# Kernel optimization log

Measured on AMD Instinct MI355X. Metric: run time of the kernel, lower is better.

Reference implementation:

```python
import jax, jax.numpy as jnp
import numpy as np
from jax import lax

H, I, N, R, K, B, L = 2048, 4096, 16, 128, 4, 1, 2048

def silu(v):
    return v * jax.nn.sigmoid(v)

def setup_inputs() -> dict:
    key = jax.random.key(0)
    ks = jax.random.split(key, 8)
    f = jnp.float32
    x = jax.random.normal(ks[0], (B, L, H), f)
    W_in = jax.random.normal(ks[1], (H, 2 * I), f) / np.sqrt(H).astype(np.float32)
    conv_w = jax.random.normal(ks[2], (I, 1, K), f) / np.sqrt(K).astype(np.float32)  # OIH depthwise
    conv_b = jnp.zeros((I,), f)
    W_x = jax.random.normal(ks[3], (I, R + 2 * N), f) / np.sqrt(I).astype(np.float32)
    W_dt = jax.random.normal(ks[4], (R, I), f) / np.sqrt(R).astype(np.float32)
    # dt bias init as in Mamba: inverse-softplus of log-uniform dt
    dt = jnp.clip(jnp.exp(jax.random.normal(ks[5], (I,), f) * (np.log(0.1) - np.log(0.001)).astype(np.float32) + np.float32(np.log(0.001))), 1e-4, 0.1)
    b_dt = dt + jnp.log(-jnp.expm1(-dt))
    W_out = jax.random.normal(ks[6], (I, H), f) / np.sqrt(I).astype(np.float32)
    A_log = jnp.log(jnp.broadcast_to(jnp.arange(1, N + 1, dtype=f), (I, N)))
    D = jnp.ones((I,), f)
    return {"x": x, "W_in": W_in, "conv_w": conv_w, "conv_b": conv_b, "W_x": W_x,
            "W_dt": W_dt, "b_dt": b_dt, "W_out": W_out, "A_log": A_log, "D": D}

def reference(x, W_in, conv_w, conv_b, W_x, W_dt, b_dt, W_out, A_log, D):
    Bsz, Lq, _ = x.shape
    proj = jnp.swapaxes(x @ W_in, 1, 2)            # [B, 2I, L]
    h, gate = jnp.split(proj, 2, axis=1)           # each [B, I, L]
    # depthwise causal conv1d (pad K-1 both sides, truncate to L)
    h = lax.conv_general_dilated(h, conv_w, (1,), ((K - 1, K - 1),), feature_group_count=I)[..., :Lq]
    h = silu(h + conv_b[None, :, None])            # [B, I, L]
    ssm = jnp.swapaxes(h, 1, 2) @ W_x              # [B, L, R+2N]
    dt, Bm, Cm = jnp.split(ssm, [R, R + N], axis=-1)
    dt = jax.nn.softplus(dt @ W_dt + b_dt)         # [B, L, I]
    dt = jnp.swapaxes(dt, 1, 2)                    # [B, I, L]
    A = -jnp.exp(A_log)                            # [I, N]
    dA = jnp.exp(A[None, :, None, :] * dt[..., None])          # [B, I, L, N]
    dBu = dt[..., None] * Bm[:, None, :, :] * h[..., None]     # [B, I, L, N]

    def step(s, inp):
        dA_t, dBu_t, C_t = inp                     # [B,I,N],[B,I,N],[B,N]
        s = dA_t * s + dBu_t
        y = jnp.einsum('bin,bn->bi', s, C_t)
        return s, y

    s0 = jnp.zeros((Bsz, I, N), x.dtype)
    _, ys = lax.scan(step, s0, (jnp.moveaxis(dA, 2, 0), jnp.moveaxis(dBu, 2, 0), jnp.swapaxes(Cm, 0, 1)))
    y = jnp.moveaxis(ys, 0, 2)                     # [B, I, L]
    y = (y + h * D[None, :, None]) * silu(gate)
    return jnp.swapaxes(y, 1, 2) @ W_out           # [B, L, H]
```

## Files before the change

kernel.cpp:

```cpp
#include <hip/hip_runtime.h>

typedef unsigned short u16;
typedef unsigned int u32;
typedef __attribute__((ext_vector_type(2))) float f32x2;
typedef __attribute__((ext_vector_type(4))) float f32x4;
typedef __attribute__((ext_vector_type(8))) short s16x8;
typedef __attribute__((ext_vector_type(4))) u16 u16x4;

static constexpr int Hdim = 2048, Idim = 4096, Ndim = 16, Rdim = 128, Lseq = 2048;
static constexpr int NCH = 64, LCH = 32;

__device__ __forceinline__ u16 f2bf(float f) {
  u32 u = __builtin_bit_cast(u32, f);
  u += 0x7fffu + ((u >> 16) & 1u);
  return (u16)(u >> 16);
}
__device__ __forceinline__ float bf2f(u16 u) {
  u32 x = ((u32)u) << 16;
  return __builtin_bit_cast(float, x);
}

__global__ void k_cvt(const float* __restrict__ src, u16* __restrict__ dst, int n4) {
  int i = blockIdx.x * blockDim.x + threadIdx.x;
  if (i >= n4) return;
  f32x4 v = ((const f32x4*)src)[i];
  u16x4 o = {f2bf(v.x), f2bf(v.y), f2bf(v.z), f2bf(v.w)};
  ((u16x4*)dst)[i] = o;
}

__global__ void k_tcvt(const float* __restrict__ src, u16* __restrict__ dst,
                       int R, int C, int dstld) {
  __shared__ float tile[32][33];
  int tx = threadIdx.x & 31, ty = threadIdx.x >> 5;
  int c0 = blockIdx.x * 32, r0 = blockIdx.y * 32;
#pragma unroll
  for (int j = 0; j < 32; j += 8) {
    int r = r0 + ty + j, c = c0 + tx;
    tile[ty + j][tx] = (r < R && c < C) ? src[(size_t)r * C + c] : 0.f;
  }
  __syncthreads();
#pragma unroll
  for (int j = 0; j < 32; j += 8) {
    int c = c0 + ty + j, r = r0 + tx;
    if (c < C && r < R) dst[(size_t)c * dstld + r] = f2bf(tile[tx][ty + j]);
  }
}

__global__ __launch_bounds__(256)
void k_tcvt64(const float* __restrict__ src, u16* __restrict__ dst, int C, int ld) {
  __shared__ u16 tile[64][68];
  const int c0 = blockIdx.x * 64, r0 = blockIdx.y * 64;
#pragma unroll
  for (int it = 0; it < 4; ++it) {
    int v = it * 256 + threadIdx.x;
    int row = v >> 4, c4 = v & 15;
    f32x4 d = *(const f32x4*)&src[(size_t)(r0 + row) * C + c0 + c4 * 4];
    u16x4 o = {f2bf(d.x), f2bf(d.y), f2bf(d.z), f2bf(d.w)};
    *(u16x4*)&tile[row][c4 * 4] = o;
  }
  __syncthreads();
#pragma unroll
  for (int it = 0; it < 4; ++it) {
    int v = it * 256 + threadIdx.x;
    int oc = v >> 4, r4 = v & 15;
    u16x4 o = {tile[r4 * 4 + 0][oc], tile[r4 * 4 + 1][oc],
               tile[r4 * 4 + 2][oc], tile[r4 * 4 + 3][oc]};
    *(u16x4*)&dst[(size_t)(c0 + oc) * ld + r0 + r4 * 4] = o;
  }
}

__global__ void k_conv(const u16* __restrict__ projb, const float* __restrict__ cw,
                       const float* __restrict__ cb, u16* __restrict__ hcb) {
  int idx = blockIdx.x * 256 + threadIdx.x;
  int i = idx & (Idim - 1), l = idx >> 12;
  float acc = cb[i];
#pragma unroll
  for (int k = 0; k < 4; ++k) {
    int lk = l - 3 + k;
    if (lk >= 0) acc += cw[i * 4 + k] * bf2f(projb[(size_t)lk * (2 * Idim) + i]);
  }
  float s = acc * (1.f / (1.f + __expf(-acc)));
  hcb[idx] = f2bf(s);
}

__global__ void k_dtr(const float* __restrict__ ssm, u16* __restrict__ dtr) {
  int i = blockIdx.x * blockDim.x + threadIdx.x;
  int l = i >> 5, c4 = i & 31;
  f32x4 v = *(const f32x4*)&ssm[(size_t)l * 256 + c4 * 4];
  u16x4 o = {f2bf(v.x), f2bf(v.y), f2bf(v.z), f2bf(v.w)};
  *(u16x4*)&dtr[(size_t)l * 128 + c4 * 4] = o;
}

__global__ __launch_bounds__(256)
void k_scan1(const float* __restrict__ dtf, const u16* __restrict__ hcb,
             const float* __restrict__ ssm, const float* __restrict__ A_log,
             float* __restrict__ Sloc, float* __restrict__ dtsum) {
  __shared__ float Bs[LCH][16];
  const int c = blockIdx.y;
  const int i = blockIdx.x * 256 + threadIdx.x;
  const int l0 = c * LCH;
  {
    int t = threadIdx.x;
    int l = t >> 3, q = t & 7;
    *(f32x2*)&Bs[l][q * 2] = *(const f32x2*)&ssm[(size_t)(l0 + l) * 256 + 128 + q * 2];
  }
  float a[16];
#pragma unroll
  for (int n4 = 0; n4 < 4; ++n4) {
    f32x4 v = *(const f32x4*)&A_log[(size_t)i * 16 + n4 * 4];
    a[n4 * 4 + 0] = -__expf(v.x);
    a[n4 * 4 + 1] = -__expf(v.y);
    a[n4 * 4 + 2] = -__expf(v.z);
    a[n4 * 4 + 3] = -__expf(v.w);
  }
  __syncthreads();
  float s[16];
#pragma unroll
  for (int n = 0; n < 16; ++n) s[n] = 0.f;
  float dsum = 0.f;
  for (int l = 0; l < LCH; ++l) {
    float dtv = dtf[(size_t)(l0 + l) * Idim + i];
    float hv = bf2f(hcb[(size_t)(l0 + l) * Idim + i]);
    dsum += dtv;
    float dh = dtv * hv;
#pragma unroll
    for (int n = 0; n < 16; ++n) {
      float dA = __expf(a[n] * dtv);
      s[n] = dA * s[n] + dh * Bs[l][n];
    }
  }
#pragma unroll
  for (int n4 = 0; n4 < 4; ++n4) {
    f32x4 v = {s[n4 * 4], s[n4 * 4 + 1], s[n4 * 4 + 2], s[n4 * 4 + 3]};
    *(f32x4*)&Sloc[((size_t)c * Idim + i) * 16 + n4 * 4] = v;
  }
  dtsum[(size_t)c * Idim + i] = dsum;
}

__global__ __launch_bounds__(256)
void k_scan2(const float* __restrict__ Sloc, const float* __restrict__ dtsum,
             const float* __restrict__ A_log, float* __restrict__ sinit) {
  const int idx = blockIdx.x * 256 + threadIdx.x;
  const float a = -__expf(A_log[idx]);
  const int i = idx >> 4;
  float acc = 0.f;
  for (int c = 0; c < NCH; ++c) {
    size_t o = (size_t)c * (Idim * 16) + idx;
    sinit[o] = acc;
    acc = __expf(a * dtsum[(size_t)c * Idim + i]) * acc + Sloc[o];
  }
}

__global__ __launch_bounds__(256)
void k_scan3(const float* __restrict__ dtf, const u16* __restrict__ hcb,
             const float* __restrict__ ssm, const float* __restrict__ A_log,
             const float* __restrict__ Dp, const u16* __restrict__ projb,
             const float* __restrict__ sinit, u16* __restrict__ yb) {
  __shared__ float SBC[LCH][32];
  const int c = blockIdx.y;
  const int i = blockIdx.x * 256 + threadIdx.x;
  const int l0 = c * LCH;
  {
    int t = threadIdx.x;
    int l = t >> 3, q = t & 7;
    *(f32x4*)&SBC[l][q * 4] = *(const f32x4*)&ssm[(size_t)(l0 + l) * 256 + 128 + q * 4];
  }
  float a[16], s[16];
#pragma unroll
  for (int n4 = 0; n4 < 4; ++n4) {
    f32x4 v = *(const f32x4*)&A_log[(size_t)i * 16 + n4 * 4];
    a[n4 * 4 + 0] = -__expf(v.x);
    a[n4 * 4 + 1] = -__expf(v.y);
    a[n4 * 4 + 2] = -__expf(v.z);
    a[n4 * 4 + 3] = -__expf(v.w);
    f32x4 sv = *(const f32x4*)&sinit[((size_t)c * Idim + i) * 16 + n4 * 4];
    s[n4 * 4 + 0] = sv.x;
    s[n4 * 4 + 1] = sv.y;
    s[n4 * 4 + 2] = sv.z;
    s[n4 * 4 + 3] = sv.w;
  }
  const float Di = Dp[i];
  __syncthreads();
  for (int l = 0; l < LCH; ++l) {
    float dtv = dtf[(size_t)(l0 + l) * Idim + i];
    float hv = bf2f(hcb[(size_t)(l0 + l) * Idim + i]);
    float dh = dtv * hv;
    float y = 0.f;
#pragma unroll
    for (int n = 0; n < 16; ++n) {
      float dA = __expf(a[n] * dtv);
      s[n] = dA * s[n] + dh * SBC[l][n];
      y += s[n] * SBC[l][16 + n];
    }
    float g = bf2f(projb[(size_t)(l0 + l) * (2 * Idim) + Idim + i]);
    y = (y + hv * Di) * (g / (1.f + __expf(-g)));
    yb[(size_t)(l0 + l) * Idim + i] = f2bf(y);
  }
}

__device__ __forceinline__ void gload_lds16(const void* g, void* l) {
  __builtin_amdgcn_global_load_lds((const __attribute__((address_space(1))) void*)g,
                                   (__attribute__((address_space(3))) void*)l, 16, 0, 0);
}

template <int EPI>
__device__ __forceinline__ void gemm_body(const u16* __restrict__ A, const u16* __restrict__ Bt,
                                          float* __restrict__ C, u16* __restrict__ Caux,
                                          int N, int K, int kchunk,
                                          const float* __restrict__ bias,
                                          int m0, int n0, int kz) {
  __shared__ u16 As[128 * 32];
  __shared__ u16 Bs[128 * 32];
  const int tid = threadIdx.x;
  const int wave = tid >> 6, lane = tid & 63;
  const int wm = (wave >> 1) * 64, wn = (wave & 1) * 64;
  const int lr = lane >> 2;
  const int lc = lane & 3;
  const int arow = wave * 32;

  f32x4 acc[4][4];
#pragma unroll
  for (int a = 0; a < 4; ++a)
#pragma unroll
    for (int b = 0; b < 4; ++b) acc[a][b] = (f32x4){0.f, 0.f, 0.f, 0.f};

  const int k_begin = kz * kchunk;
  const int k_end = k_begin + kchunk;

  for (int k = k_begin; k < k_end; k += 32) {
#pragma unroll
    for (int j = 0; j < 2; ++j) {
      const u16* ga = A + (size_t)(m0 + arow + j * 16 + lr) * K + k + lc * 8;
      gload_lds16(ga, &As[(arow + j * 16) * 32]);
      const u16* gb = Bt + (size_t)(n0 + arow + j * 16 + lr) * K + k + lc * 8;
      gload_lds16(gb, &Bs[(arow + j * 16) * 32]);
    }
    __syncthreads();
    const int kh = (lane >> 4) * 8;
    const int fr = lane & 15;
    s16x8 af[4], bfr[4];
#pragma unroll
    for (int f = 0; f < 4; ++f) {
      af[f] = *(const s16x8*)&As[(wm + f * 16 + fr) * 32 + kh];
      bfr[f] = *(const s16x8*)&Bs[(wn + f * 16 + fr) * 32 + kh];
    }
#pragma unroll
    for (int fm = 0; fm < 4; ++fm)
#pragma unroll
      for (int fn = 0; fn < 4; ++fn)
        acc[fm][fn] = __builtin_amdgcn_mfma_f32_16x16x32_bf16(af[fm], bfr[fn], acc[fm][fn], 0, 0, 0);
    __syncthreads();
  }

  const int cr = (lane >> 4) * 4, cc = lane & 15;
#pragma unroll
  for (int fm = 0; fm < 4; ++fm)
#pragma unroll
    for (int fn = 0; fn < 4; ++fn)
#pragma unroll
      for (int j = 0; j < 4; ++j) {
        int row = m0 + wm + fm * 16 + cr + j;
        int col = n0 + wn + fn * 16 + cc;
        float v = acc[fm][fn][j];
        if (EPI == 0) {
          C[(size_t)row * N + col] = v;
        } else if (EPI == 1) {
          atomicAdd(&C[(size_t)row * N + col], v);
        } else if (EPI == 2) {
          float xv = v + bias[col];
          C[(size_t)row * N + col] = fmaxf(xv, 0.f) + log1pf(__expf(-fabsf(xv)));
        } else {
          Caux[(size_t)row * N + col] = f2bf(v);
        }
      }
}

__global__ __launch_bounds__(256)
void k_gemm1(const u16* __restrict__ A, const u16* __restrict__ Bt, u16* __restrict__ Caux) {
  int bid = blockIdx.x;
  int wg = (bid & 7) * 128 + (bid >> 3);
  int m0 = (wg & 15) * 128, n0 = (wg >> 4) * 128;
  gemm_body<4>(A, Bt, nullptr, Caux, 2 * Idim, Hdim, Hdim, nullptr, m0, n0, 0);
}

__global__ __launch_bounds__(256)
void k_gemm3(const u16* __restrict__ A, const u16* __restrict__ Bt, float* __restrict__ C) {
  gemm_body<1>(A, Bt, C, nullptr, 256, Idim, Idim / 8, nullptr,
               blockIdx.x * 128, blockIdx.y * 128, blockIdx.z);
}

__global__ __launch_bounds__(256)
void k_gemm4(const u16* __restrict__ A, const u16* __restrict__ Bt, float* __restrict__ C,
             const float* __restrict__ bias) {
  gemm_body<2>(A, Bt, C, nullptr, Idim, Rdim, Rdim, bias,
               blockIdx.x * 128, blockIdx.y * 128, 0);
}

__global__ __launch_bounds__(256)
void k_gemm5(const u16* __restrict__ A, const u16* __restrict__ Bt, float* __restrict__ C) {
  int bid = blockIdx.x;
  int wg = (bid & 7) * 32 + (bid >> 3);
  int m0 = (wg & 15) * 128, n0 = (wg >> 4) * 128;
  gemm_body<1>(A, Bt, C, nullptr, Hdim, Idim, Idim / 2, nullptr, m0, n0, blockIdx.y);
}

extern "C" void kernel_launch(void* const* d_in, const int* in_sizes, int n_in,
                              void* d_out, int out_size, void* d_ws, size_t ws_size,
                              hipStream_t stream) {
  const float* x = (const float*)d_in[0];
  const float* W_in = (const float*)d_in[1];
  const float* convw = (const float*)d_in[2];
  const float* convb = (const float*)d_in[3];
  const float* W_x = (const float*)d_in[4];
  const float* W_dt = (const float*)d_in[5];
  const float* b_dt = (const float*)d_in[6];
  const float* W_out = (const float*)d_in[7];
  const float* A_log = (const float*)d_in[8];
  const float* Dp = (const float*)d_in[9];
  float* out = (float*)d_out;

  char* w = (char*)d_ws;
  const size_t OFF_PROJ = 0;
  const size_t OFF_HC = OFF_PROJ + (size_t)Lseq * 2 * Idim * 4;
  const size_t OFF_DT = OFF_HC + (size_t)Lseq * Idim * 4;
  const size_t OFF_XB = OFF_DT + (size_t)Lseq * Idim * 4;
  const size_t OFF_WIN = OFF_XB + (size_t)Lseq * Hdim * 2;
  const size_t OFF_WOUT = OFF_WIN + (size_t)2 * Idim * Hdim * 2;
  const size_t OFF_HCB = OFF_WOUT + (size_t)Hdim * Idim * 2;
  const size_t OFF_YB = OFF_HCB + (size_t)Lseq * Idim * 2;
  const size_t OFF_WX = OFF_YB + (size_t)Lseq * Idim * 2;
  const size_t OFF_WDT = OFF_WX + (size_t)256 * Idim * 2;
  const size_t OFF_SSM = OFF_WDT + (size_t)Idim * Rdim * 2;
  const size_t OFF_DTR = OFF_SSM + (size_t)Lseq * 256 * 4;

  u16* projb = (u16*)(w + OFF_PROJ);
  float* dtf = (float*)(w + OFF_DT);
  u16* xb = (u16*)(w + OFF_XB);
  u16* winT = (u16*)(w + OFF_WIN);
  u16* woutT = (u16*)(w + OFF_WOUT);
  u16* hcb = (u16*)(w + OFF_HCB);
  u16* yb = (u16*)(w + OFF_YB);
  u16* wxt = (u16*)(w + OFF_WX);
  u16* wdtT = (u16*)(w + OFF_WDT);
  float* ssm = (float*)(w + OFF_SSM);
  u16* dtr = (u16*)(w + OFF_DTR);
  float* Sloc = (float*)(w + OFF_HC);
  float* sinit = (float*)(w + OFF_WIN);
  float* dtsum = (float*)(w + OFF_WIN + (size_t)16 * 1024 * 1024);

  hipMemsetAsync(wxt, 0, (size_t)256 * Idim * 2, stream);
  hipMemsetAsync(ssm, 0, (size_t)Lseq * 256 * 4, stream);
  hipMemsetAsync(out, 0, (size_t)Lseq * Hdim * 4, stream);

  k_cvt<<<(Lseq * Hdim / 4 + 255) / 256, 256, 0, stream>>>(x, xb, Lseq * Hdim / 4);
  k_tcvt64<<<dim3(2 * Idim / 64, Hdim / 64), 256, 0, stream>>>(W_in, winT, 2 * Idim, Hdim);
  k_tcvt<<<dim3(5, Idim / 32), 256, 0, stream>>>(W_x, wxt, Idim, 160, Idim);
  k_tcvt64<<<dim3(Idim / 64, Rdim / 64), 256, 0, stream>>>(W_dt, wdtT, Idim, Rdim);
  k_tcvt64<<<dim3(Hdim / 64, Idim / 64), 256, 0, stream>>>(W_out, woutT, Hdim, Idim);

  k_gemm1<<<1024, 256, 0, stream>>>(xb, winT, projb);

  k_conv<<<(size_t)Lseq * Idim / 256, 256, 0, stream>>>(projb, convw, convb, hcb);

  k_gemm3<<<dim3(Lseq / 128, 2, 8), 256, 0, stream>>>(hcb, wxt, ssm);

  k_dtr<<<Lseq * 32 / 256, 256, 0, stream>>>(ssm, dtr);

  k_gemm4<<<dim3(Lseq / 128, Idim / 128), 256, 0, stream>>>(dtr, wdtT, dtf, b_dt);

  k_scan1<<<dim3(Idim / 256, NCH), 256, 0, stream>>>(dtf, hcb, ssm, A_log, Sloc, dtsum);
  k_scan2<<<Idim * 16 / 256, 256, 0, stream>>>(Sloc, dtsum, A_log, sinit);
  k_scan3<<<dim3(Idim / 256, NCH), 256, 0, stream>>>(dtf, hcb, ssm, A_log, Dp, projb, sinit, yb);

  k_gemm5<<<dim3(256, 2), 256, 0, stream>>>(yb, woutT, out);
}
```

Baseline: 514.0 us.

## Replace input-projection GEMM with 256x256 eight-wave pipelined kernel; store dt as bf16

Replaces the 128x128 input-projection GEMM with a 512-thread, 256x256-tile kernel. It uses 128 KB of dynamic LDS, double-buffered half-tile staging via global_load_lds, interleaved barriers and MFMA priority hints, so loads overlap compute and operands are reused more. It also makes the dt projection epilogue write softplus output as bf16, and the scan kernels read it as bf16, halving that traffic at some precision cost. Two memsets are merged into one covering the contiguous W_x and ssm regions.

```diff
diff --git a/kernel.cpp b/kernel.cpp
--- a/kernel.cpp
+++ b/kernel.cpp
@@ -92,7 +92,7 @@
 }
 
 __global__ __launch_bounds__(256)
-void k_scan1(const float* __restrict__ dtf, const u16* __restrict__ hcb,
+void k_scan1(const u16* __restrict__ dtfb, const u16* __restrict__ hcb,
              const float* __restrict__ ssm, const float* __restrict__ A_log,
              float* __restrict__ Sloc, float* __restrict__ dtsum) {
   __shared__ float Bs[LCH][16];
@@ -119,7 +119,7 @@
   for (int n = 0; n < 16; ++n) s[n] = 0.f;
   float dsum = 0.f;
   for (int l = 0; l < LCH; ++l) {
-    float dtv = dtf[(size_t)(l0 + l) * Idim + i];
+    float dtv = bf2f(dtfb[(size_t)(l0 + l) * Idim + i]);
     float hv = bf2f(hcb[(size_t)(l0 + l) * Idim + i]);
     dsum += dtv;
     float dh = dtv * hv;
@@ -152,7 +152,7 @@
 }
 
 __global__ __launch_bounds__(256)
-void k_scan3(const float* __restrict__ dtf, const u16* __restrict__ hcb,
+void k_scan3(const u16* __restrict__ dtfb, const u16* __restrict__ hcb,
              const float* __restrict__ ssm, const float* __restrict__ A_log,
              const float* __restrict__ Dp, const u16* __restrict__ projb,
              const float* __restrict__ sinit, u16* __restrict__ yb) {
@@ -182,7 +182,7 @@
   const float Di = Dp[i];
   __syncthreads();
   for (int l = 0; l < LCH; ++l) {
-    float dtv = dtf[(size_t)(l0 + l) * Idim + i];
+    float dtv = bf2f(dtfb[(size_t)(l0 + l) * Idim + i]);
     float hv = bf2f(hcb[(size_t)(l0 + l) * Idim + i]);
     float dh = dtv * hv;
     float y = 0.f;
@@ -262,25 +262,13 @@
         int row = m0 + wm + fm * 16 + cr + j;
         int col = n0 + wn + fn * 16 + cc;
         float v = acc[fm][fn][j];
-        if (EPI == 0) {
-          C[(size_t)row * N + col] = v;
-        } else if (EPI == 1) {
+        if (EPI == 1) {
           atomicAdd(&C[(size_t)row * N + col], v);
-        } else if (EPI == 2) {
+        } else {
           float xv = v + bias[col];
-          C[(size_t)row * N + col] = fmaxf(xv, 0.f) + log1pf(__expf(-fabsf(xv)));
-        } else {
-          Caux[(size_t)row * N + col] = f2bf(v);
+          Caux[(size_t)row * N + col] = f2bf(fmaxf(xv, 0.f) + log1pf(__expf(-fabsf(xv))));
         }
       }
-}
-
-__global__ __launch_bounds__(256)
-void k_gemm1(const u16* __restrict__ A, const u16* __restrict__ Bt, u16* __restrict__ Caux) {
-  int bid = blockIdx.x;
-  int wg = (bid & 7) * 128 + (bid >> 3);
-  int m0 = (wg & 15) * 128, n0 = (wg >> 4) * 128;
-  gemm_body<4>(A, Bt, nullptr, Caux, 2 * Idim, Hdim, Hdim, nullptr, m0, n0, 0);
 }
 
 __global__ __launch_bounds__(256)
@@ -290,9 +278,9 @@
 }
 
 __global__ __launch_bounds__(256)
-void k_gemm4(const u16* __restrict__ A, const u16* __restrict__ Bt, float* __restrict__ C,
+void k_gemm4(const u16* __restrict__ A, const u16* __restrict__ Bt, u16* __restrict__ Caux,
              const float* __restrict__ bias) {
-  gemm_body<2>(A, Bt, C, nullptr, Idim, Rdim, Rdim, bias,
+  gemm_body<5>(A, Bt, nullptr, Caux, Idim, Rdim, Rdim, bias,
                blockIdx.x * 128, blockIdx.y * 128, 0);
 }
 
@@ -302,6 +290,157 @@
   int wg = (bid & 7) * 32 + (bid >> 3);
   int m0 = (wg & 15) * 128, n0 = (wg >> 4) * 128;
   gemm_body<1>(A, Bt, C, nullptr, Hdim, Idim, Idim / 2, nullptr, m0, n0, blockIdx.y);
+}
+
+static constexpr int G1K = 2048;
+static constexpr int G1NT = G1K / 64;
+static constexpr int G1NITER = G1NT / 2;
+
+__device__ __forceinline__ void g1_stage(const u16* __restrict__ g, int ld, int row0, int kcol,
+                                         u16* lds, int slot, int wid, int lane) {
+#pragma unroll
+  for (int j = 0; j < 2; ++j) {
+    const u16* ga = g + (size_t)(row0 + j * 64 + wid * 8 + (lane >> 3)) * ld
+                      + kcol + (((lane & 7) ^ (lane >> 3)) << 3);
+    gload_lds16(ga, &lds[slot + j * 4096 + wid * 512]);
+  }
+}
+
+#define ASLOT(buf, h) (((buf)*2 + (h)) * 8192)
+#define BSLOT(buf, h) (32768 + ((buf)*2 + (h)) * 8192)
+
+template <int BUF, int MH, int NH>
+__device__ __forceinline__ void g1_compute(const u16* lds, f32x4 (&acc)[2][4][2][2],
+                                           int qm, int qn, int lane) {
+  const int r16 = lane & 15, kq = lane >> 4;
+  s16x8 af[4][2], bq[2][2];
+#pragma unroll
+  for (int fm = 0; fm < 4; ++fm) {
+    int row = qm * 64 + fm * 16 + r16;
+#pragma unroll
+    for (int ks = 0; ks < 2; ++ks) {
+      int ch = (ks * 4 + kq) ^ (row & 7);
+      af[fm][ks] = *(const s16x8*)&lds[ASLOT(BUF, MH) + row * 64 + ch * 8];
+    }
+  }
+#pragma unroll
+  for (int fn = 0; fn < 2; ++fn) {
+    int row = qn * 32 + fn * 16 + r16;
+#pragma unroll
+    for (int ks = 0; ks < 2; ++ks) {
+      int ch = (ks * 4 + kq) ^ (row & 7);
+      bq[fn][ks] = *(const s16x8*)&lds[BSLOT(BUF, NH) + row * 64 + ch * 8];
+    }
+  }
+  __builtin_amdgcn_s_setprio(1);
+#pragma unroll
+  for (int fm = 0; fm < 4; ++fm)
+#pragma unroll
+    for (int fn = 0; fn < 2; ++fn)
+#pragma unroll
+      for (int ks = 0; ks < 2; ++ks)
+        acc[MH][fm][NH][fn] =
+            __builtin_amdgcn_mfma_f32_16x16x32_bf16(af[fm][ks], bq[fn][ks], acc[MH][fm][NH][fn], 0, 0, 0);
+  __builtin_amdgcn_s_setprio(0);
+}
+
+#define G1BAR()                         \
+  do {                                  \
+    __builtin_amdgcn_s_barrier();       \
+    __builtin_amdgcn_sched_barrier(0);  \
+  } while (0)
+#define G1VM4() asm volatile("s_waitcnt vmcnt(4)" ::: "memory")
+
+__global__ __launch_bounds__(512, 2)
+void k_gemm1_8p(const u16* __restrict__ A, const u16* __restrict__ Bt, u16* __restrict__ Cb) {
+  extern __shared__ u16 lds[];
+  const int tid = threadIdx.x, wid = tid >> 6, lane = tid & 63;
+  const int qm = wid >> 2, qn = wid & 3;
+  const int m0 = (int)(blockIdx.x >> 5) * 256, n0 = (int)(blockIdx.x & 31) * 256;
+
+  f32x4 acc[2][4][2][2];
+#pragma unroll
+  for (int a = 0; a < 2; ++a)
+#pragma unroll
+    for (int b = 0; b < 4; ++b)
+#pragma unroll
+      for (int c = 0; c < 2; ++c)
+#pragma unroll
+        for (int d = 0; d < 2; ++d) acc[a][b][c][d] = (f32x4){0.f, 0.f, 0.f, 0.f};
+
+  g1_stage(A, G1K, m0, 0, lds, ASLOT(0, 0), wid, lane);
+  g1_stage(Bt, G1K, n0 + 128, 0, lds, BSLOT(0, 1), wid, lane);
+  g1_stage(A, G1K, m0 + 128, 0, lds, ASLOT(0, 1), wid, lane);
+  g1_stage(Bt, G1K, n0, 0, lds, BSLOT(0, 0), wid, lane);
+  g1_stage(A, G1K, m0, 64, lds, ASLOT(1, 0), wid, lane);
+  g1_stage(Bt, G1K, n0 + 128, 64, lds, BSLOT(1, 1), wid, lane);
+
+  for (int i = 0; i < G1NITER - 1; ++i) {
+    const int kc0 = i * 128, kc2 = kc0 + 128, kc3 = kc0 + 192;
+    g1_stage(A, G1K, m0 + 128, kc0 + 64, lds, ASLOT(1, 1), wid, lane);
+    G1VM4();
+    G1BAR();
+    g1_compute<0, 0, 0>(lds, acc, qm, qn, lane);
+    G1BAR();
+    g1_stage(Bt, G1K, n0, kc0 + 64, lds, BSLOT(1, 0), wid, lane);
+    G1BAR();
+    g1_compute<0, 0, 1>(lds, acc, qm, qn, lane);
+    G1BAR();
+    g1_stage(A, G1K, m0, kc2, lds, ASLOT(0, 0), wid, lane);
+    G1BAR();
+    g1_compute<0, 1, 1>(lds, acc, qm, qn, lane);
+    G1BAR();
+    g1_stage(Bt, G1K, n0 + 128, kc2, lds, BSLOT(0, 1), wid, lane);
+    G1BAR();
+    g1_compute<0, 1, 0>(lds, acc, qm, qn, lane);
+    G1BAR();
+    g1_stage(A, G1K, m0 + 128, kc2, lds, ASLOT(0, 1), wid, lane);
+    G1VM4();
+    G1BAR();
+    g1_compute<1, 0, 0>(lds, acc, qm, qn, lane);
+    G1BAR();
+    g1_stage(Bt, G1K, n0, kc2, lds, BSLOT(0, 0), wid, lane);
+    G1BAR();
+    g1_compute<1, 0, 1>(lds, acc, qm, qn, lane);
+    G1BAR();
+    g1_stage(A, G1K, m0, kc3, lds, ASLOT(1, 0), wid, lane);
+    G1BAR();
+    g1_compute<1, 1, 1>(lds, acc, qm, qn, lane);
+    G1BAR();
+    g1_stage(Bt, G1K, n0 + 128, kc3, lds, BSLOT(1, 1), wid, lane);
+    G1BAR();
+    g1_compute<1, 1, 0>(lds, acc, qm, qn, lane);
+    G1BAR();
+  }
+
+  g1_stage(A, G1K, m0 + 128, (G1NT - 1) * 64, lds, ASLOT(1, 1), wid, lane);
+  g1_stage(Bt, G1K, n0, (G1NT - 1) * 64, lds, BSLOT(1, 0), wid, lane);
+  asm volatile("s_waitcnt vmcnt(0)" ::: "memory");
+  G1BAR();
+  g1_compute<0, 0, 0>(lds, acc, qm, qn, lane);
+  g1_compute<0, 0, 1>(lds, acc, qm, qn, lane);
+  g1_compute<0, 1, 1>(lds, acc, qm, qn, lane);
+  g1_compute<0, 1, 0>(lds, acc, qm, qn, lane);
+  g1_compute<1, 0, 0>(lds, acc, qm, qn, lane);
+  g1_compute<1, 0, 1>(lds, acc, qm, qn, lane);
+  g1_compute<1, 1, 1>(lds, acc, qm, qn, lane);
+  g1_compute<1, 1, 0>(lds, acc, qm, qn, lane);
+
+  const int cr = (lane >> 4) * 4, cc = lane & 15;
+#pragma unroll
+  for (int mh = 0; mh < 2; ++mh)
+#pragma unroll
+    for (int fm = 0; fm < 4; ++fm)
+#pragma unroll
+      for (int nh = 0; nh < 2; ++nh)
+#pragma unroll
+        for (int fn = 0; fn < 2; ++fn)
+#pragma unroll
+          for (int j = 0; j < 4; ++j) {
+            int row = m0 + mh * 128 + qm * 64 + fm * 16 + cr + j;
+            int col = n0 + nh * 128 + qn * 32 + fn * 16 + cc;
+            Cb[(size_t)row * 8192 + col] = f2bf(acc[mh][fm][nh][fn][j]);
+          }
 }
 
 extern "C" void kernel_launch(void* const* d_in, const int* in_sizes, int n_in,
@@ -334,7 +473,7 @@
   const size_t OFF_DTR = OFF_SSM + (size_t)Lseq * 256 * 4;
 
   u16* projb = (u16*)(w + OFF_PROJ);
-  float* dtf = (float*)(w + OFF_DT);
+  u16* dtfb = (u16*)(w + OFF_DT);
   u16* xb = (u16*)(w + OFF_XB);
   u16* winT = (u16*)(w + OFF_WIN);
   u16* woutT = (u16*)(w + OFF_WOUT);
@@ -348,8 +487,7 @@
   float* sinit = (float*)(w + OFF_WIN);
   float* dtsum = (float*)(w + OFF_WIN + (size_t)16 * 1024 * 1024);
 
-  hipMemsetAsync(wxt, 0, (size_t)256 * Idim * 2, stream);
-  hipMemsetAsync(ssm, 0, (size_t)Lseq * 256 * 4, stream);
+  hipMemsetAsync(wxt, 0, (size_t)(OFF_SSM - OFF_WX) + (size_t)Lseq * 256 * 4, stream);
   hipMemsetAsync(out, 0, (size_t)Lseq * Hdim * 4, stream);
 
   k_cvt<<<(Lseq * Hdim / 4 + 255) / 256, 256, 0, stream>>>(x, xb, Lseq * Hdim / 4);
@@ -358,7 +496,8 @@
   k_tcvt64<<<dim3(Idim / 64, Rdim / 64), 256, 0, stream>>>(W_dt, wdtT, Idim, Rdim);
   k_tcvt64<<<dim3(Hdim / 64, Idim / 64), 256, 0, stream>>>(W_out, woutT, Hdim, Idim);
 
-  k_gemm1<<<1024, 256, 0, stream>>>(xb, winT, projb);
+  hipFuncSetAttribute((const void*)k_gemm1_8p, hipFuncAttributeMaxDynamicSharedMemorySize, 131072);
+  k_gemm1_8p<<<256, 512, 131072, stream>>>(xb, winT, projb);
 
   k_conv<<<(size_t)Lseq * Idim / 256, 256, 0, stream>>>(projb, convw, convb, hcb);
 
@@ -366,11 +505,11 @@
 
   k_dtr<<<Lseq * 32 / 256, 256, 0, stream>>>(ssm, dtr);
 
-  k_gemm4<<<dim3(Lseq / 128, Idim / 128), 256, 0, stream>>>(dtr, wdtT, dtf, b_dt);
-
-  k_scan1<<<dim3(Idim / 256, NCH), 256, 0, stream>>>(dtf, hcb, ssm, A_log, Sloc, dtsum);
+  k_gemm4<<<dim3(Lseq / 128, Idim / 128), 256, 0, stream>>>(dtr, wdtT, dtfb, b_dt);
+
+  k_scan1<<<dim3(Idim / 256, NCH), 256, 0, stream>>>(dtfb, hcb, ssm, A_log, Sloc, dtsum);
   k_scan2<<<Idim * 16 / 256, 256, 0, stream>>>(Sloc, dtsum, A_log, sinit);
-  k_scan3<<<dim3(Idim / 256, NCH), 256, 0, stream>>>(dtf, hcb, ssm, A_log, Dp, projb, sinit, yb);
+  k_scan3<<<dim3(Idim / 256, NCH), 256, 0, stream>>>(dtfb, hcb, ssm, A_log, Dp, projb, sinit, yb);
 
   k_gemm5<<<dim3(256, 2), 256, 0, stream>>>(yb, woutT, out);
 }
```

Measured after the change: 480.5 us. 6.5% less time.
